# Kernel optimization log

Measured on AMD Instinct MI355X. Metric: run time of the kernel, lower is better.

Reference implementation:

```python
import jax, jax.numpy as jnp
import numpy as np

B, T, D, U = 2048, 200, 128, 128  # batch, history len, input dim, gru units


def setup_inputs() -> dict:
    key = jax.random.key(0)
    ks = jax.random.split(key, 5)
    s = 1.0 / np.sqrt(U + D)
    return {
        "history_state": jax.random.normal(ks[0], (B, T, D), jnp.float32),
        "attention_score": jax.random.uniform(ks[1], (B, T, 1), jnp.float32),
        "Wu": jax.random.normal(ks[2], (U + D, U), jnp.float32) * s,
        "bu": jnp.zeros((U,), jnp.float32),
        "Wr": jax.random.normal(ks[3], (U + D, U), jnp.float32) * s,
        "br": jnp.zeros((U,), jnp.float32),
        "Wh": jax.random.normal(ks[4], (D + U, U), jnp.float32) * s,
        "bh": jnp.zeros((U,), jnp.float32),
    }


def reference(history_state, attention_score, Wu, bu, Wr, br, Wh, bh):
    # time-major for scan: (T, B, ...)
    xs = jnp.swapaxes(history_state, 0, 1)       # (T, B, D)
    ats = jnp.swapaxes(attention_score, 0, 1)    # (T, B, 1)
    h0 = jnp.zeros((history_state.shape[0], Wu.shape[1]), history_state.dtype)

    def step(h, xa):
        x, a = xa
        hx = jnp.concatenate([h, x], axis=-1)                       # (B, U+D)
        u = jax.nn.sigmoid(hx @ Wu + bu)                            # update gate
        r = jax.nn.sigmoid(hx @ Wr + br)                            # reset gate
        hh = jnp.tanh(jnp.concatenate([x, r * h], axis=-1) @ Wh + bh)
        u = u * a                                                   # attention-modulated update
        h_new = u * hh + (1.0 - u) * h
        return h_new, None

    h_final, _ = jax.lax.scan(step, h0, (xs, ats))
    return h_final  # (B, U)
```

## Files before the change

### kernel.cpp

```cpp
#include <hip/hip_runtime.h>
#include <hip/hip_bf16.h>


#define T_LEN 200
#define D_DIM 128
#define U_DIM 128
#define BM    16
#define KCS   136
#define XSTEP (16 * KCS)

typedef __attribute__((ext_vector_type(8))) short bf16x8;
typedef __attribute__((ext_vector_type(4))) float f32x4;
typedef __attribute__((ext_vector_type(4))) unsigned int uint4v;

#define MFMA __builtin_amdgcn_mfma_f32_16x16x32_bf16

static __device__ __forceinline__ unsigned short f2bf(float f) {
    unsigned int u = __builtin_bit_cast(unsigned int, f);
    u += 0x7fffu + ((u >> 16) & 1u);
    return (unsigned short)(u >> 16);
}
static __device__ __forceinline__ unsigned int pkbf2(float a, float b) {
    float2 t; t.x = a; t.y = b;
    __hip_bfloat162 v = __float22bfloat162_rn(t);
    unsigned int u; __builtin_memcpy(&u, &v, 4);
    return u;
}
static __device__ __forceinline__ bf16x8 pack8bf(f32x4 lo, f32x4 hi) {
    uint4v v;
    v[0] = pkbf2(lo[0], lo[1]); v[1] = pkbf2(lo[2], lo[3]);
    v[2] = pkbf2(hi[0], hi[1]); v[3] = pkbf2(hi[2], hi[3]);
    return __builtin_bit_cast(bf16x8, v);
}
static __device__ __forceinline__ float fast_exp2(float x) {
#if __has_builtin(__builtin_amdgcn_exp2f)
    return __builtin_amdgcn_exp2f(x);
#else
    return exp2f(x);
#endif
}
static __device__ __forceinline__ float fast_rcp(float x) {
#if __has_builtin(__builtin_amdgcn_rcpf)
    return __builtin_amdgcn_rcpf(x);
#else
    return 1.0f / x;
#endif
}
static __device__ __forceinline__ void block_sync_lds() {
    asm volatile("s_waitcnt lgkmcnt(0)" ::: "memory");
    __builtin_amdgcn_sched_barrier(0);
    __builtin_amdgcn_s_barrier();
    __builtin_amdgcn_sched_barrier(0);
}

__global__ __launch_bounds__(256, 1)
void gru_scan_kernel(const float* __restrict__ X,
                     const float* __restrict__ Att,
                     const float* __restrict__ Wu, const float* __restrict__ bu,
                     const float* __restrict__ Wr, const float* __restrict__ br,
                     const float* __restrict__ Wh, const float* __restrict__ bh,
                     float* __restrict__ out)
{
    __shared__ __align__(16) unsigned short h_bf[XSTEP];
    __shared__ __align__(16) unsigned short rh_bf[XSTEP];

    const int tid  = threadIdx.x;
    const int wave = tid >> 6;
    const int lane = tid & 63;
    const int q    = lane >> 4;
    const int ln   = lane & 15;
    const int b0   = blockIdx.x * BM;

    const float INVLN2 = 1.4426950408889634f;

    bf16x8 wu[2][8], wr[2][8], wh[2][8];
    f32x4 nbu[2], nbr[2], bh2[2];
    #pragma unroll
    for (int tl = 0; tl < 2; ++tl) {
        const int tb = 32 * wave + 16 * tl;
        const int c  = tb + ln;
        const f32x4 bu4 = *(const f32x4*)&bu[tb + 4 * q];
        const f32x4 br4 = *(const f32x4*)&br[tb + 4 * q];
        const f32x4 bh4 = *(const f32x4*)&bh[tb + 4 * q];
        #pragma unroll
        for (int r = 0; r < 4; ++r) {
            nbu[tl][r] = -bu4[r] * INVLN2;
            nbr[tl][r] = -br4[r] * INVLN2;
            bh2[tl][r] = 2.0f * bh4[r] * INVLN2;
        }
        #pragma unroll
        for (int kt = 0; kt < 8; ++kt) {
            const int k0 = 32 * kt + 8 * q;
            bf16x8 vu, vr, vh;
            #pragma unroll
            for (int j = 0; j < 8; ++j) {
                vu[j] = (short)f2bf(Wu[(k0 + j) * U_DIM + c] * -INVLN2);
                vr[j] = (short)f2bf(Wr[(k0 + j) * U_DIM + c] * -INVLN2);
                vh[j] = (short)f2bf(Wh[(k0 + j) * U_DIM + c] * (2.0f * INVLN2));
            }
            wu[tl][kt] = vu; wr[tl][kt] = vr; wh[tl][kt] = vh;
        }
    }

    const float* xrow = X + (size_t)(b0 + ln) * T_LEN * D_DIM + 8 * q;
    const float* arow = Att + (size_t)(b0 + ln) * T_LEN;

    f32x4 px[8];
    #pragma unroll
    for (int kt = 0; kt < 4; ++kt) {
        px[2 * kt]     = *(const f32x4*)(xrow + 32 * kt);
        px[2 * kt + 1] = *(const f32x4*)(xrow + 32 * kt + 4);
    }
    const float a0 = arow[0];
    float attA = arow[1], attB = arow[2], attC = arow[3];

    float hreg[2][4];

    const int c8base = (4 * wave) * KCS + ln * 8 + (q & 1) * 4;
    const int c8q    = (q >> 1) * KCS;

    {
        bf16x8 xf[4];
        #pragma unroll
        for (int kt = 0; kt < 4; ++kt) xf[kt] = pack8bf(px[2 * kt], px[2 * kt + 1]);
        #pragma unroll
        for (int kt = 0; kt < 4; ++kt) {
            px[2 * kt]     = *(const f32x4*)(xrow + D_DIM + 32 * kt);
            px[2 * kt + 1] = *(const f32x4*)(xrow + D_DIM + 32 * kt + 4);
        }
        #pragma unroll
        for (int tl = 0; tl < 2; ++tl) {
            f32x4 xu = nbu[tl], xh = bh2[tl];
            #pragma unroll
            for (int kt = 0; kt < 4; ++kt) {
                xu = MFMA(wu[tl][kt + 4], xf[kt], xu, 0, 0, 0);
                xh = MFMA(wh[tl][kt],     xf[kt], xh, 0, 0, 0);
            }
            #pragma unroll
            for (int r = 0; r < 4; ++r) {
                float u  = fast_rcp(1.0f + fast_exp2(xu[r])) * a0;
                float hh = 1.0f - 2.0f * fast_rcp(1.0f + fast_exp2(xh[r]));
                hreg[tl][r] = u * hh;
            }
            uint2 wv; wv.x = pkbf2(hreg[tl][0], hreg[tl][1]);
            wv.y = pkbf2(hreg[tl][2], hreg[tl][3]);
            *(uint2*)&h_bf[c8base + c8q + 2 * tl * KCS] = wv;
        }
    }
    block_sync_lds();

    for (int t = 1; t < T_LEN; ++t) {
        bf16x8 hf[4];
        #pragma unroll
        for (int kt = 0; kt < 4; ++kt)
            hf[kt] = *(const bf16x8*)&h_bf[(4 * kt + q) * KCS + ln * 8];

        bf16x8 xf[4];
        #pragma unroll
        for (int kt = 0; kt < 4; ++kt) xf[kt] = pack8bf(px[2 * kt], px[2 * kt + 1]);
        {
            const int tn = (t + 1 < T_LEN) ? t + 1 : T_LEN - 1;
            const float* xs = xrow + (size_t)tn * D_DIM;
            #pragma unroll
            for (int kt = 0; kt < 4; ++kt) {
                px[2 * kt]     = *(const f32x4*)(xs + 32 * kt);
                px[2 * kt + 1] = *(const f32x4*)(xs + 32 * kt + 4);
            }
        }
        const float a_att = attA;
        attA = attB; attB = attC;
        attC = arow[(t + 3 < T_LEN) ? t + 3 : T_LEN - 1];

        f32x4 xr[2], xu[2], xh[2];
        #pragma unroll
        for (int tl = 0; tl < 2; ++tl) {
            xr[tl] = nbr[tl]; xu[tl] = nbu[tl]; xh[tl] = bh2[tl];
            #pragma unroll
            for (int kt = 0; kt < 4; ++kt) {
                xr[tl] = MFMA(wr[tl][kt + 4], xf[kt], xr[tl], 0, 0, 0);
                xu[tl] = MFMA(wu[tl][kt + 4], xf[kt], xu[tl], 0, 0, 0);
                xh[tl] = MFMA(wh[tl][kt],     xf[kt], xh[tl], 0, 0, 0);
            }
        }
        f32x4 ra[2], rb[2];
        #pragma unroll
        for (int tl = 0; tl < 2; ++tl) {
            ra[tl] = MFMA(wr[tl][0], hf[0], (f32x4)0.0f, 0, 0, 0);
            rb[tl] = MFMA(wr[tl][2], hf[2], (f32x4)0.0f, 0, 0, 0);
            ra[tl] = MFMA(wr[tl][1], hf[1], ra[tl], 0, 0, 0);
            rb[tl] = MFMA(wr[tl][3], hf[3], rb[tl], 0, 0, 0);
            #pragma unroll
            for (int kt = 0; kt < 4; ++kt)
                xu[tl] = MFMA(wu[tl][kt], hf[kt], xu[tl], 0, 0, 0);
        }
        #pragma unroll
        for (int tl = 0; tl < 2; ++tl) {
            float rh[4];
            #pragma unroll
            for (int r = 0; r < 4; ++r) {
                float zr = xr[tl][r] + ra[tl][r] + rb[tl][r];
                float rv = fast_rcp(1.0f + fast_exp2(zr));
                rh[r] = rv * hreg[tl][r];
            }
            uint2 wv; wv.x = pkbf2(rh[0], rh[1]); wv.y = pkbf2(rh[2], rh[3]);
            *(uint2*)&rh_bf[c8base + c8q + 2 * tl * KCS] = wv;
        }
        block_sync_lds();

        bf16x8 rf[4];
        #pragma unroll
        for (int kt = 0; kt < 4; ++kt)
            rf[kt] = *(const bf16x8*)&rh_bf[(4 * kt + q) * KCS + ln * 8];

        float uq[2][4];
        #pragma unroll
        for (int tl = 0; tl < 2; ++tl)
            #pragma unroll
            for (int r = 0; r < 4; ++r)
                uq[tl][r] = fast_rcp(1.0f + fast_exp2(xu[tl][r])) * a_att;

        #pragma unroll
        for (int tl = 0; tl < 2; ++tl) {
            f32x4 ha = xh[tl], hb = (f32x4)0.0f;
            ha = MFMA(wh[tl][4], rf[0], ha, 0, 0, 0);
            hb = MFMA(wh[tl][6], rf[2], hb, 0, 0, 0);
            ha = MFMA(wh[tl][5], rf[1], ha, 0, 0, 0);
            hb = MFMA(wh[tl][7], rf[3], hb, 0, 0, 0);
            #pragma unroll
            for (int r = 0; r < 4; ++r) {
                float z  = ha[r] + hb[r];
                float hh = 1.0f - 2.0f * fast_rcp(1.0f + fast_exp2(z));
                float ho = hreg[tl][r];
                hreg[tl][r] = ho + uq[tl][r] * (hh - ho);
            }
            uint2 wv; wv.x = pkbf2(hreg[tl][0], hreg[tl][1]);
            wv.y = pkbf2(hreg[tl][2], hreg[tl][3]);
            *(uint2*)&h_bf[c8base + c8q + 2 * tl * KCS] = wv;
        }
        block_sync_lds();
    }

    #pragma unroll
    for (int tl = 0; tl < 2; ++tl) {
        f32x4 v;
        #pragma unroll
        for (int r = 0; r < 4; ++r) v[r] = hreg[tl][r];
        *(f32x4*)&out[(size_t)(b0 + ln) * U_DIM + 32 * wave + 16 * tl + 4 * q] = v;
    }
}

extern "C" void kernel_launch(void* const* d_in, const int* in_sizes, int n_in,
                              void* d_out, int out_size, void* d_ws, size_t ws_size,
                              hipStream_t stream) {
    const float* X   = (const float*)d_in[0];
    const float* Att = (const float*)d_in[1];
    const float* Wu  = (const float*)d_in[2];
    const float* bu  = (const float*)d_in[3];
    const float* Wr  = (const float*)d_in[4];
    const float* br  = (const float*)d_in[5];
    const float* Wh  = (const float*)d_in[6];
    const float* bh  = (const float*)d_in[7];
    float* out = (float*)d_out;

    gru_scan_kernel<<<dim3(2048 / BM), dim3(256), 0, stream>>>(
        X, Att, Wu, bu, Wr, br, Wh, bh, out);
}
```

Measured before the change: 538.1 us.

## Split GRU units across eight waves and pipeline x-projection into previous step

Each block now launches 512 threads (8 waves), and each wave owns 16 output units instead of 32. That halves per-wave weight registers and MFMA work per step, so the critical serial path inside each timestep is shorter. The input projection for the next step (x@W plus bias) is computed after the h update and before the barrier, which moves it off the h-dependent critical path. In exchange the block has twice as many waves taking part in each barrier, and occupancy targets change with the launch bounds.

```diff
diff --git a/kernel.cpp b/kernel.cpp
--- a/kernel.cpp
+++ b/kernel.cpp
@@ -53,7 +53,7 @@
     __builtin_amdgcn_sched_barrier(0);
 }
 
-__global__ __launch_bounds__(256, 1)
+__global__ __launch_bounds__(512, 2)
 void gru_scan_kernel(const float* __restrict__ X,
                      const float* __restrict__ Att,
                      const float* __restrict__ Wu, const float* __restrict__ bu,
@@ -73,20 +73,19 @@
 
     const float INVLN2 = 1.4426950408889634f;
 
-    bf16x8 wu[2][8], wr[2][8], wh[2][8];
-    f32x4 nbu[2], nbr[2], bh2[2];
-    #pragma unroll
-    for (int tl = 0; tl < 2; ++tl) {
-        const int tb = 32 * wave + 16 * tl;
+    bf16x8 wu[8], wr[8], wh[8];
+    f32x4 nbu, nbr, bh2;
+    {
+        const int tb = 16 * wave;
         const int c  = tb + ln;
         const f32x4 bu4 = *(const f32x4*)&bu[tb + 4 * q];
         const f32x4 br4 = *(const f32x4*)&br[tb + 4 * q];
         const f32x4 bh4 = *(const f32x4*)&bh[tb + 4 * q];
         #pragma unroll
         for (int r = 0; r < 4; ++r) {
-            nbu[tl][r] = -bu4[r] * INVLN2;
-            nbr[tl][r] = -br4[r] * INVLN2;
-            bh2[tl][r] = 2.0f * bh4[r] * INVLN2;
+            nbu[r] = -bu4[r] * INVLN2;
+            nbr[r] = -br4[r] * INVLN2;
+            bh2[r] = 2.0f * bh4[r] * INVLN2;
         }
         #pragma unroll
         for (int kt = 0; kt < 8; ++kt) {
@@ -98,7 +97,7 @@
                 vr[j] = (short)f2bf(Wr[(k0 + j) * U_DIM + c] * -INVLN2);
                 vh[j] = (short)f2bf(Wh[(k0 + j) * U_DIM + c] * (2.0f * INVLN2));
             }
-            wu[tl][kt] = vu; wr[tl][kt] = vr; wh[tl][kt] = vh;
+            wu[kt] = vu; wr[kt] = vr; wh[kt] = vh;
         }
     }
 
@@ -114,10 +113,10 @@
     const float a0 = arow[0];
     float attA = arow[1], attB = arow[2], attC = arow[3];
 
-    float hreg[2][4];
-
-    const int c8base = (4 * wave) * KCS + ln * 8 + (q & 1) * 4;
-    const int c8q    = (q >> 1) * KCS;
+    float hreg[4];
+    f32x4 acc_r, acc_u, acc_h;
+
+    const int c8 = (2 * wave + (q >> 1)) * KCS + ln * 8 + (q & 1) * 4;
 
     {
         bf16x8 xf[4];
@@ -128,23 +127,36 @@
             px[2 * kt]     = *(const f32x4*)(xrow + D_DIM + 32 * kt);
             px[2 * kt + 1] = *(const f32x4*)(xrow + D_DIM + 32 * kt + 4);
         }
-        #pragma unroll
-        for (int tl = 0; tl < 2; ++tl) {
-            f32x4 xu = nbu[tl], xh = bh2[tl];
-            #pragma unroll
-            for (int kt = 0; kt < 4; ++kt) {
-                xu = MFMA(wu[tl][kt + 4], xf[kt], xu, 0, 0, 0);
-                xh = MFMA(wh[tl][kt],     xf[kt], xh, 0, 0, 0);
-            }
-            #pragma unroll
-            for (int r = 0; r < 4; ++r) {
-                float u  = fast_rcp(1.0f + fast_exp2(xu[r])) * a0;
-                float hh = 1.0f - 2.0f * fast_rcp(1.0f + fast_exp2(xh[r]));
-                hreg[tl][r] = u * hh;
-            }
-            uint2 wv; wv.x = pkbf2(hreg[tl][0], hreg[tl][1]);
-            wv.y = pkbf2(hreg[tl][2], hreg[tl][3]);
-            *(uint2*)&h_bf[c8base + c8q + 2 * tl * KCS] = wv;
+        f32x4 xu = nbu, xh = bh2;
+        #pragma unroll
+        for (int kt = 0; kt < 4; ++kt) {
+            xu = MFMA(wu[kt + 4], xf[kt], xu, 0, 0, 0);
+            xh = MFMA(wh[kt],     xf[kt], xh, 0, 0, 0);
+        }
+        #pragma unroll
+        for (int r = 0; r < 4; ++r) {
+            float u  = fast_rcp(1.0f + fast_exp2(xu[r])) * a0;
+            float hh = 1.0f - 2.0f * fast_rcp(1.0f + fast_exp2(xh[r]));
+            hreg[r] = u * hh;
+        }
+        {
+            uint2 wv; wv.x = pkbf2(hreg[0], hreg[1]); wv.y = pkbf2(hreg[2], hreg[3]);
+            *(uint2*)&h_bf[c8] = wv;
+        }
+        bf16x8 x1[4];
+        #pragma unroll
+        for (int kt = 0; kt < 4; ++kt) x1[kt] = pack8bf(px[2 * kt], px[2 * kt + 1]);
+        #pragma unroll
+        for (int kt = 0; kt < 4; ++kt) {
+            px[2 * kt]     = *(const f32x4*)(xrow + 2 * D_DIM + 32 * kt);
+            px[2 * kt + 1] = *(const f32x4*)(xrow + 2 * D_DIM + 32 * kt + 4);
+        }
+        acc_r = nbr; acc_u = nbu; acc_h = bh2;
+        #pragma unroll
+        for (int kt = 0; kt < 4; ++kt) {
+            acc_r = MFMA(wr[kt + 4], x1[kt], acc_r, 0, 0, 0);
+            acc_u = MFMA(wu[kt + 4], x1[kt], acc_u, 0, 0, 0);
+            acc_h = MFMA(wh[kt],     x1[kt], acc_h, 0, 0, 0);
         }
     }
     block_sync_lds();
@@ -155,97 +167,87 @@
         for (int kt = 0; kt < 4; ++kt)
             hf[kt] = *(const bf16x8*)&h_bf[(4 * kt + q) * KCS + ln * 8];
 
-        bf16x8 xf[4];
-        #pragma unroll
-        for (int kt = 0; kt < 4; ++kt) xf[kt] = pack8bf(px[2 * kt], px[2 * kt + 1]);
-        {
-            const int tn = (t + 1 < T_LEN) ? t + 1 : T_LEN - 1;
+        f32x4 ra = acc_r, rb = (f32x4)0.0f;
+        ra = MFMA(wr[0], hf[0], ra, 0, 0, 0);
+        rb = MFMA(wr[2], hf[2], rb, 0, 0, 0);
+        ra = MFMA(wr[1], hf[1], ra, 0, 0, 0);
+        rb = MFMA(wr[3], hf[3], rb, 0, 0, 0);
+        #pragma unroll
+        for (int kt = 0; kt < 4; ++kt)
+            acc_u = MFMA(wu[kt], hf[kt], acc_u, 0, 0, 0);
+
+        {
+            float rh[4];
+            #pragma unroll
+            for (int r = 0; r < 4; ++r) {
+                float zr = ra[r] + rb[r];
+                float rv = fast_rcp(1.0f + fast_exp2(zr));
+                rh[r] = rv * hreg[r];
+            }
+            uint2 wv; wv.x = pkbf2(rh[0], rh[1]); wv.y = pkbf2(rh[2], rh[3]);
+            *(uint2*)&rh_bf[c8] = wv;
+        }
+        block_sync_lds();
+
+        bf16x8 rf[4];
+        #pragma unroll
+        for (int kt = 0; kt < 4; ++kt)
+            rf[kt] = *(const bf16x8*)&rh_bf[(4 * kt + q) * KCS + ln * 8];
+
+        const float a_att = attA;
+        attA = attB; attB = attC;
+        attC = arow[(t + 3 < T_LEN) ? t + 3 : T_LEN - 1];
+        float uq[4];
+        #pragma unroll
+        for (int r = 0; r < 4; ++r)
+            uq[r] = fast_rcp(1.0f + fast_exp2(acc_u[r])) * a_att;
+
+        f32x4 ha = acc_h, hb = (f32x4)0.0f;
+        ha = MFMA(wh[4], rf[0], ha, 0, 0, 0);
+        hb = MFMA(wh[6], rf[2], hb, 0, 0, 0);
+        ha = MFMA(wh[5], rf[1], ha, 0, 0, 0);
+        hb = MFMA(wh[7], rf[3], hb, 0, 0, 0);
+
+        #pragma unroll
+        for (int r = 0; r < 4; ++r) {
+            float z  = ha[r] + hb[r];
+            float hh = 1.0f - 2.0f * fast_rcp(1.0f + fast_exp2(z));
+            float ho = hreg[r];
+            hreg[r] = ho + uq[r] * (hh - ho);
+        }
+        {
+            uint2 wv; wv.x = pkbf2(hreg[0], hreg[1]); wv.y = pkbf2(hreg[2], hreg[3]);
+            *(uint2*)&h_bf[c8] = wv;
+        }
+
+        {
+            bf16x8 xf[4];
+            #pragma unroll
+            for (int kt = 0; kt < 4; ++kt)
+                xf[kt] = pack8bf(px[2 * kt], px[2 * kt + 1]);
+            const int tn = (t + 2 < T_LEN) ? t + 2 : T_LEN - 1;
             const float* xs = xrow + (size_t)tn * D_DIM;
             #pragma unroll
             for (int kt = 0; kt < 4; ++kt) {
                 px[2 * kt]     = *(const f32x4*)(xs + 32 * kt);
                 px[2 * kt + 1] = *(const f32x4*)(xs + 32 * kt + 4);
             }
-        }
-        const float a_att = attA;
-        attA = attB; attB = attC;
-        attC = arow[(t + 3 < T_LEN) ? t + 3 : T_LEN - 1];
-
-        f32x4 xr[2], xu[2], xh[2];
-        #pragma unroll
-        for (int tl = 0; tl < 2; ++tl) {
-            xr[tl] = nbr[tl]; xu[tl] = nbu[tl]; xh[tl] = bh2[tl];
+            acc_r = nbr; acc_u = nbu; acc_h = bh2;
             #pragma unroll
             for (int kt = 0; kt < 4; ++kt) {
-                xr[tl] = MFMA(wr[tl][kt + 4], xf[kt], xr[tl], 0, 0, 0);
-                xu[tl] = MFMA(wu[tl][kt + 4], xf[kt], xu[tl], 0, 0, 0);
-                xh[tl] = MFMA(wh[tl][kt],     xf[kt], xh[tl], 0, 0, 0);
-            }
-        }
-        f32x4 ra[2], rb[2];
-        #pragma unroll
-        for (int tl = 0; tl < 2; ++tl) {
-            ra[tl] = MFMA(wr[tl][0], hf[0], (f32x4)0.0f, 0, 0, 0);
-            rb[tl] = MFMA(wr[tl][2], hf[2], (f32x4)0.0f, 0, 0, 0);
-            ra[tl] = MFMA(wr[tl][1], hf[1], ra[tl], 0, 0, 0);
-            rb[tl] = MFMA(wr[tl][3], hf[3], rb[tl], 0, 0, 0);
-            #pragma unroll
-            for (int kt = 0; kt < 4; ++kt)
-                xu[tl] = MFMA(wu[tl][kt], hf[kt], xu[tl], 0, 0, 0);
-        }
-        #pragma unroll
-        for (int tl = 0; tl < 2; ++tl) {
-            float rh[4];
-            #pragma unroll
-            for (int r = 0; r < 4; ++r) {
-                float zr = xr[tl][r] + ra[tl][r] + rb[tl][r];
-                float rv = fast_rcp(1.0f + fast_exp2(zr));
-                rh[r] = rv * hreg[tl][r];
-            }
-            uint2 wv; wv.x = pkbf2(rh[0], rh[1]); wv.y = pkbf2(rh[2], rh[3]);
-            *(uint2*)&rh_bf[c8base + c8q + 2 * tl * KCS] = wv;
+                acc_r = MFMA(wr[kt + 4], xf[kt], acc_r, 0, 0, 0);
+                acc_u = MFMA(wu[kt + 4], xf[kt], acc_u, 0, 0, 0);
+                acc_h = MFMA(wh[kt],     xf[kt], acc_h, 0, 0, 0);
+            }
         }
         block_sync_lds();
-
-        bf16x8 rf[4];
-        #pragma unroll
-        for (int kt = 0; kt < 4; ++kt)
-            rf[kt] = *(const bf16x8*)&rh_bf[(4 * kt + q) * KCS + ln * 8];
-
-        float uq[2][4];
-        #pragma unroll
-        for (int tl = 0; tl < 2; ++tl)
-            #pragma unroll
-            for (int r = 0; r < 4; ++r)
-                uq[tl][r] = fast_rcp(1.0f + fast_exp2(xu[tl][r])) * a_att;
-
-        #pragma unroll
-        for (int tl = 0; tl < 2; ++tl) {
-            f32x4 ha = xh[tl], hb = (f32x4)0.0f;
-            ha = MFMA(wh[tl][4], rf[0], ha, 0, 0, 0);
-            hb = MFMA(wh[tl][6], rf[2], hb, 0, 0, 0);
-            ha = MFMA(wh[tl][5], rf[1], ha, 0, 0, 0);
-            hb = MFMA(wh[tl][7], rf[3], hb, 0, 0, 0);
-            #pragma unroll
-            for (int r = 0; r < 4; ++r) {
-                float z  = ha[r] + hb[r];
-                float hh = 1.0f - 2.0f * fast_rcp(1.0f + fast_exp2(z));
-                float ho = hreg[tl][r];
-                hreg[tl][r] = ho + uq[tl][r] * (hh - ho);
-            }
-            uint2 wv; wv.x = pkbf2(hreg[tl][0], hreg[tl][1]);
-            wv.y = pkbf2(hreg[tl][2], hreg[tl][3]);
-            *(uint2*)&h_bf[c8base + c8q + 2 * tl * KCS] = wv;
-        }
-        block_sync_lds();
-    }
-
-    #pragma unroll
-    for (int tl = 0; tl < 2; ++tl) {
+    }
+
+    {
         f32x4 v;
         #pragma unroll
-        for (int r = 0; r < 4; ++r) v[r] = hreg[tl][r];
-        *(f32x4*)&out[(size_t)(b0 + ln) * U_DIM + 32 * wave + 16 * tl + 4 * q] = v;
+        for (int r = 0; r < 4; ++r) v[r] = hreg[r];
+        *(f32x4*)&out[(size_t)(b0 + ln) * U_DIM + 16 * wave + 4 * q] = v;
     }
 }
 
@@ -262,6 +264,6 @@
     const float* bh  = (const float*)d_in[7];
     float* out = (float*)d_out;
 
-    gru_scan_kernel<<<dim3(2048 / BM), dim3(256), 0, stream>>>(
+    gru_scan_kernel<<<dim3(2048 / BM), dim3(512), 0, stream>>>(
         X, Att, Wu, bu, Wr, br, Wh, bh, out);
 }
```

Measured after the change: 682.7 us. +26.9%, slower.

## Add producer waves that stage X chunks into LDS as bf16 for compute waves

Applied to the files above, without the earlier changes.

Splits the block into 4 compute waves and 4 producer waves. The producer waves load X and attention in 12-step chunks, convert them to bf16 and write them into a double-buffered LDS area. The compute waves then read x fragments from LDS, and the input projection for step s+1 is computed at the end of step s so it sits off the critical path. This removes per-step global loads and packing from the recurrent loop. The cost is more LDS, 512 threads per block with launch bounds of 2 blocks, and producer waves that must join every barrier.

```diff
diff --git a/kernel.cpp b/kernel.cpp
--- a/kernel.cpp
+++ b/kernel.cpp
@@ -6,6 +6,8 @@
 #define D_DIM 128
 #define U_DIM 128
 #define BM    16
+#define CH    12
+#define NCH   ((T_LEN + CH - 1) / CH)
 #define KCS   136
 #define XSTEP (16 * KCS)
 
@@ -26,11 +28,11 @@
     unsigned int u; __builtin_memcpy(&u, &v, 4);
     return u;
 }
-static __device__ __forceinline__ bf16x8 pack8bf(f32x4 lo, f32x4 hi) {
+static __device__ __forceinline__ uint4v pack8u(float4 lo, float4 hi) {
     uint4v v;
-    v[0] = pkbf2(lo[0], lo[1]); v[1] = pkbf2(lo[2], lo[3]);
-    v[2] = pkbf2(hi[0], hi[1]); v[3] = pkbf2(hi[2], hi[3]);
-    return __builtin_bit_cast(bf16x8, v);
+    v[0] = pkbf2(lo.x, lo.y); v[1] = pkbf2(lo.z, lo.w);
+    v[2] = pkbf2(hi.x, hi.y); v[3] = pkbf2(hi.z, hi.w);
+    return v;
 }
 static __device__ __forceinline__ float fast_exp2(float x) {
 #if __has_builtin(__builtin_amdgcn_exp2f)
@@ -53,7 +55,40 @@
     __builtin_amdgcn_sched_barrier(0);
 }
 
-__global__ __launch_bounds__(256, 1)
+#define XPART(SRC) do {                                                        \
+    bf16x8 xf_[4];                                                             \
+    _Pragma("unroll")                                                          \
+    for (int kt = 0; kt < 4; ++kt)                                             \
+        xf_[kt] = *(const bf16x8*)&(SRC)[(4 * kt + q) * KCS + ln * 8];         \
+    _Pragma("unroll")                                                          \
+    for (int tl = 0; tl < 2; ++tl) {                                           \
+        acc_r[tl] = nbr[tl]; acc_u[tl] = nbu[tl]; acc_h[tl] = bh2[tl];         \
+        _Pragma("unroll")                                                      \
+        for (int kt = 0; kt < 4; ++kt) {                                       \
+            acc_r[tl] = MFMA(wr[tl][kt + 4], xf_[kt], acc_r[tl], 0, 0, 0);     \
+            acc_u[tl] = MFMA(wu[tl][kt + 4], xf_[kt], acc_u[tl], 0, 0, 0);     \
+            acc_h[tl] = MFMA(wh[tl][kt],     xf_[kt], acc_h[tl], 0, 0, 0);     \
+        }                                                                      \
+    }                                                                          \
+} while (0)
+
+#define P_ISSUE(PX, SB) do {                                                   \
+    _Pragma("unroll")                                                          \
+    for (int k = 0; k < 4; ++k) {                                              \
+        int t_ = tn0 + (SB) + k; t_ = (t_ < T_LEN) ? t_ : (T_LEN - 1);         \
+        const float* src_ = xb + (size_t)t_ * D_DIM;                           \
+        (PX)[2 * k]     = *(const float4*)(src_);                              \
+        (PX)[2 * k + 1] = *(const float4*)(src_ + 4);                          \
+    }                                                                          \
+} while (0)
+#define P_WRITE(PX, SB) do {                                                   \
+    _Pragma("unroll")                                                          \
+    for (int k = 0; k < 4; ++k)                                                \
+        *(uint4v*)&dst[((SB) + k) * XSTEP + cs * KCS + srow * 8] =             \
+            pack8u((PX)[2 * k], (PX)[2 * k + 1]);                              \
+} while (0)
+
+__global__ __launch_bounds__(512, 2)
 void gru_scan_kernel(const float* __restrict__ X,
                      const float* __restrict__ Att,
                      const float* __restrict__ Wu, const float* __restrict__ bu,
@@ -61,8 +96,10 @@
                      const float* __restrict__ Wh, const float* __restrict__ bh,
                      float* __restrict__ out)
 {
+    __shared__ __align__(16) unsigned short x_sm[2][CH * XSTEP];
     __shared__ __align__(16) unsigned short h_bf[XSTEP];
     __shared__ __align__(16) unsigned short rh_bf[XSTEP];
+    __shared__ float a_sm[2][CH * BM];
 
     const int tid  = threadIdx.x;
     const int wave = tid >> 6;
@@ -73,179 +110,202 @@
 
     const float INVLN2 = 1.4426950408889634f;
 
-    bf16x8 wu[2][8], wr[2][8], wh[2][8];
-    f32x4 nbu[2], nbr[2], bh2[2];
-    #pragma unroll
-    for (int tl = 0; tl < 2; ++tl) {
-        const int tb = 32 * wave + 16 * tl;
-        const int c  = tb + ln;
-        const f32x4 bu4 = *(const f32x4*)&bu[tb + 4 * q];
-        const f32x4 br4 = *(const f32x4*)&br[tb + 4 * q];
-        const f32x4 bh4 = *(const f32x4*)&bh[tb + 4 * q];
+    {
+        unsigned int* hz = (unsigned int*)h_bf;
+        unsigned int* rz = (unsigned int*)rh_bf;
+        for (int i = tid; i < XSTEP / 2; i += 512) { hz[i] = 0; rz[i] = 0; }
+    }
+
+    {
+        const int s2   = tid >> 8;
+        const int srow = (tid >> 4) & 15;
+        const int cs   = tid & 15;
+        const float* xb = X + (size_t)(b0 + srow) * T_LEN * D_DIM + cs * 8;
+        float4 px[CH];
         #pragma unroll
-        for (int r = 0; r < 4; ++r) {
-            nbu[tl][r] = -bu4[r] * INVLN2;
-            nbr[tl][r] = -br4[r] * INVLN2;
-            bh2[tl][r] = 2.0f * bh4[r] * INVLN2;
-        }
+        for (int w2 = 0; w2 < CH / 2; ++w2) {
+            const int t = 2 * w2 + s2;
+            const float* src = xb + (size_t)t * D_DIM;
+            px[2 * w2]     = *(const float4*)(src);
+            px[2 * w2 + 1] = *(const float4*)(src + 4);
+        }
+        float a_px = 0.0f;
+        if (tid < BM * CH) a_px = Att[(size_t)(b0 + (tid & 15)) * T_LEN + (tid >> 4)];
         #pragma unroll
-        for (int kt = 0; kt < 8; ++kt) {
-            const int k0 = 32 * kt + 8 * q;
-            bf16x8 vu, vr, vh;
-            #pragma unroll
-            for (int j = 0; j < 8; ++j) {
-                vu[j] = (short)f2bf(Wu[(k0 + j) * U_DIM + c] * -INVLN2);
-                vr[j] = (short)f2bf(Wr[(k0 + j) * U_DIM + c] * -INVLN2);
-                vh[j] = (short)f2bf(Wh[(k0 + j) * U_DIM + c] * (2.0f * INVLN2));
-            }
-            wu[tl][kt] = vu; wr[tl][kt] = vr; wh[tl][kt] = vh;
-        }
+        for (int w2 = 0; w2 < CH / 2; ++w2) {
+            const int s = 2 * w2 + s2;
+            *(uint4v*)&x_sm[0][s * XSTEP + cs * KCS + srow * 8] =
+                pack8u(px[2 * w2], px[2 * w2 + 1]);
+        }
+        if (tid < BM * CH) a_sm[0][tid] = a_px;
     }
-
-    const float* xrow = X + (size_t)(b0 + ln) * T_LEN * D_DIM + 8 * q;
-    const float* arow = Att + (size_t)(b0 + ln) * T_LEN;
-
-    f32x4 px[8];
-    #pragma unroll
-    for (int kt = 0; kt < 4; ++kt) {
-        px[2 * kt]     = *(const f32x4*)(xrow + 32 * kt);
-        px[2 * kt + 1] = *(const f32x4*)(xrow + 32 * kt + 4);
-    }
-    const float a0 = arow[0];
-    float attA = arow[1], attB = arow[2], attC = arow[3];
-
-    float hreg[2][4];
-
-    const int c8base = (4 * wave) * KCS + ln * 8 + (q & 1) * 4;
-    const int c8q    = (q >> 1) * KCS;
-
-    {
-        bf16x8 xf[4];
-        #pragma unroll
-        for (int kt = 0; kt < 4; ++kt) xf[kt] = pack8bf(px[2 * kt], px[2 * kt + 1]);
-        #pragma unroll
-        for (int kt = 0; kt < 4; ++kt) {
-            px[2 * kt]     = *(const f32x4*)(xrow + D_DIM + 32 * kt);
-            px[2 * kt + 1] = *(const f32x4*)(xrow + D_DIM + 32 * kt + 4);
-        }
+    __syncthreads();
+
+    if (wave < 4) {
+        bf16x8 wu[2][8], wr[2][8], wh[2][8];
+        f32x4 nbu[2], nbr[2], bh2[2];
         #pragma unroll
         for (int tl = 0; tl < 2; ++tl) {
-            f32x4 xu = nbu[tl], xh = bh2[tl];
+            const int tb = 32 * wave + 16 * tl;
+            const int c  = tb + ln;
+            const f32x4 bu4 = *(const f32x4*)&bu[tb + 4 * q];
+            const f32x4 br4 = *(const f32x4*)&br[tb + 4 * q];
+            const f32x4 bh4 = *(const f32x4*)&bh[tb + 4 * q];
             #pragma unroll
-            for (int kt = 0; kt < 4; ++kt) {
-                xu = MFMA(wu[tl][kt + 4], xf[kt], xu, 0, 0, 0);
-                xh = MFMA(wh[tl][kt],     xf[kt], xh, 0, 0, 0);
+            for (int r = 0; r < 4; ++r) {
+                nbu[tl][r] = -bu4[r] * INVLN2;
+                nbr[tl][r] = -br4[r] * INVLN2;
+                bh2[tl][r] = 2.0f * bh4[r] * INVLN2;
             }
             #pragma unroll
-            for (int r = 0; r < 4; ++r) {
-                float u  = fast_rcp(1.0f + fast_exp2(xu[r])) * a0;
-                float hh = 1.0f - 2.0f * fast_rcp(1.0f + fast_exp2(xh[r]));
-                hreg[tl][r] = u * hh;
+            for (int kt = 0; kt < 8; ++kt) {
+                const int k0 = 32 * kt + 8 * q;
+                bf16x8 vu, vr, vh;
+                #pragma unroll
+                for (int j = 0; j < 8; ++j) {
+                    vu[j] = (short)f2bf(Wu[(k0 + j) * U_DIM + c] * -INVLN2);
+                    vr[j] = (short)f2bf(Wr[(k0 + j) * U_DIM + c] * -INVLN2);
+                    vh[j] = (short)f2bf(Wh[(k0 + j) * U_DIM + c] * (2.0f * INVLN2));
+                }
+                wu[tl][kt] = vu; wr[tl][kt] = vr; wh[tl][kt] = vh;
             }
-            uint2 wv; wv.x = pkbf2(hreg[tl][0], hreg[tl][1]);
-            wv.y = pkbf2(hreg[tl][2], hreg[tl][3]);
-            *(uint2*)&h_bf[c8base + c8q + 2 * tl * KCS] = wv;
-        }
-    }
-    block_sync_lds();
-
-    for (int t = 1; t < T_LEN; ++t) {
-        bf16x8 hf[4];
-        #pragma unroll
-        for (int kt = 0; kt < 4; ++kt)
-            hf[kt] = *(const bf16x8*)&h_bf[(4 * kt + q) * KCS + ln * 8];
-
-        bf16x8 xf[4];
-        #pragma unroll
-        for (int kt = 0; kt < 4; ++kt) xf[kt] = pack8bf(px[2 * kt], px[2 * kt + 1]);
-        {
-            const int tn = (t + 1 < T_LEN) ? t + 1 : T_LEN - 1;
-            const float* xs = xrow + (size_t)tn * D_DIM;
-            #pragma unroll
-            for (int kt = 0; kt < 4; ++kt) {
-                px[2 * kt]     = *(const f32x4*)(xs + 32 * kt);
-                px[2 * kt + 1] = *(const f32x4*)(xs + 32 * kt + 4);
+        }
+
+        float hreg[2][4] = {{0.f,0.f,0.f,0.f},{0.f,0.f,0.f,0.f}};
+        const int c8base = (4 * wave) * KCS + ln * 8 + (q & 1) * 4;
+        const int c8q    = (q >> 1) * KCS;
+
+        f32x4 acc_r[2], acc_u[2], acc_h[2];
+        XPART(&x_sm[0][0]);
+
+        int t0 = 0;
+        for (int ch = 0; ch < NCH; ++ch) {
+            const int L = (t0 + CH <= T_LEN) ? CH : (T_LEN - t0);
+            const unsigned short* xcur = &x_sm[ch & 1][0];
+            const float* ab = &a_sm[ch & 1][0];
+
+            for (int s = 0; s < L; ++s) {
+                bf16x8 hf[4];
+                #pragma unroll
+                for (int kt = 0; kt < 4; ++kt)
+                    hf[kt] = *(const bf16x8*)&h_bf[(4 * kt + q) * KCS + ln * 8];
+                const float a_att = ab[s * BM + ln];
+
+                f32x4 ra[2], rb[2];
+                #pragma unroll
+                for (int tl = 0; tl < 2; ++tl) {
+                    ra[tl] = acc_r[tl]; rb[tl] = (f32x4)0.0f;
+                    ra[tl] = MFMA(wr[tl][0], hf[0], ra[tl], 0, 0, 0);
+                    rb[tl] = MFMA(wr[tl][2], hf[2], rb[tl], 0, 0, 0);
+                    ra[tl] = MFMA(wr[tl][1], hf[1], ra[tl], 0, 0, 0);
+                    rb[tl] = MFMA(wr[tl][3], hf[3], rb[tl], 0, 0, 0);
+                    #pragma unroll
+                    for (int kt = 0; kt < 4; ++kt)
+                        acc_u[tl] = MFMA(wu[tl][kt], hf[kt], acc_u[tl], 0, 0, 0);
+                }
+                #pragma unroll
+                for (int tl = 0; tl < 2; ++tl) {
+                    float rh[4];
+                    #pragma unroll
+                    for (int r = 0; r < 4; ++r) {
+                        float zr = ra[tl][r] + rb[tl][r];
+                        float rv = fast_rcp(1.0f + fast_exp2(zr));
+                        rh[r] = rv * hreg[tl][r];
+                    }
+                    uint2 wv; wv.x = pkbf2(rh[0], rh[1]); wv.y = pkbf2(rh[2], rh[3]);
+                    *(uint2*)&rh_bf[c8base + c8q + 2 * tl * KCS] = wv;
+                }
+                block_sync_lds();
+
+                bf16x8 rf[4];
+                #pragma unroll
+                for (int kt = 0; kt < 4; ++kt)
+                    rf[kt] = *(const bf16x8*)&rh_bf[(4 * kt + q) * KCS + ln * 8];
+
+                float uq[2][4];
+                #pragma unroll
+                for (int tl = 0; tl < 2; ++tl)
+                    #pragma unroll
+                    for (int r = 0; r < 4; ++r)
+                        uq[tl][r] = fast_rcp(1.0f + fast_exp2(acc_u[tl][r])) * a_att;
+
+                #pragma unroll
+                for (int tl = 0; tl < 2; ++tl) {
+                    f32x4 ha = acc_h[tl], hb = (f32x4)0.0f;
+                    ha = MFMA(wh[tl][4], rf[0], ha, 0, 0, 0);
+                    hb = MFMA(wh[tl][6], rf[2], hb, 0, 0, 0);
+                    ha = MFMA(wh[tl][5], rf[1], ha, 0, 0, 0);
+                    hb = MFMA(wh[tl][7], rf[3], hb, 0, 0, 0);
+                    #pragma unroll
+                    for (int r = 0; r < 4; ++r) {
+                        float z  = ha[r] + hb[r];
+                        float hh = 1.0f - 2.0f * fast_rcp(1.0f + fast_exp2(z));
+                        float ho = hreg[tl][r];
+                        hreg[tl][r] = ho + uq[tl][r] * (hh - ho);
+                    }
+                    uint2 wv; wv.x = pkbf2(hreg[tl][0], hreg[tl][1]);
+                    wv.y = pkbf2(hreg[tl][2], hreg[tl][3]);
+                    *(uint2*)&h_bf[c8base + c8q + 2 * tl * KCS] = wv;
+                }
+
+                if (s + 1 < L) {
+                    XPART(xcur + (s + 1) * XSTEP);
+                } else if (ch + 1 < NCH) {
+                    XPART(&x_sm[(ch + 1) & 1][0]);
+                }
+                block_sync_lds();
             }
-        }
-        const float a_att = attA;
-        attA = attB; attB = attC;
-        attC = arow[(t + 3 < T_LEN) ? t + 3 : T_LEN - 1];
-
-        f32x4 xr[2], xu[2], xh[2];
+            t0 += CH;
+        }
+
         #pragma unroll
         for (int tl = 0; tl < 2; ++tl) {
-            xr[tl] = nbr[tl]; xu[tl] = nbu[tl]; xh[tl] = bh2[tl];
+            f32x4 v;
             #pragma unroll
-            for (int kt = 0; kt < 4; ++kt) {
-                xr[tl] = MFMA(wr[tl][kt + 4], xf[kt], xr[tl], 0, 0, 0);
-                xu[tl] = MFMA(wu[tl][kt + 4], xf[kt], xu[tl], 0, 0, 0);
-                xh[tl] = MFMA(wh[tl][kt],     xf[kt], xh[tl], 0, 0, 0);
+            for (int r = 0; r < 4; ++r) v[r] = hreg[tl][r];
+            *(f32x4*)&out[(size_t)(b0 + ln) * U_DIM + 32 * wave + 16 * tl + 4 * q] = v;
+        }
+    } else {
+        const int tid2 = tid & 255;
+        const int srow = (tid2 >> 4) & 15;
+        const int cs   = tid2 & 15;
+        const float* xb = X + (size_t)(b0 + srow) * T_LEN * D_DIM + cs * 8;
+
+        int t0 = 0;
+        for (int ch = 0; ch < NCH; ++ch) {
+            const int L = (t0 + CH <= T_LEN) ? CH : (T_LEN - t0);
+            const bool st = (ch + 1 < NCH);
+            const int tn0 = t0 + CH;
+            unsigned short* dst = &x_sm[(ch + 1) & 1][0];
+            float4 pxA[8], pxB[8], pxC[8];
+            float av = 0.0f;
+
+            for (int s = 0; s < L; ++s) {
+                if (st && s == 0) {
+                    P_ISSUE(pxA, 0);
+                    if (tid2 < BM * CH) {
+                        int ta = tn0 + (tid2 >> 4);
+                        ta = (ta < T_LEN) ? ta : (T_LEN - 1);
+                        av = Att[(size_t)(b0 + (tid2 & 15)) * T_LEN + ta];
+                    }
+                }
+                block_sync_lds();
+                if (st) {
+                    if (s == 1) {
+                        P_WRITE(pxA, 0);
+                        P_ISSUE(pxB, 4);
+                        if (tid2 < BM * CH) a_sm[(ch + 1) & 1][tid2] = av;
+                    } else if (s == 2) {
+                        P_WRITE(pxB, 4);
+                        P_ISSUE(pxC, 8);
+                    } else if (s == 3) {
+                        P_WRITE(pxC, 8);
+                    }
+                }
+                block_sync_lds();
             }
-        }
-        f32x4 ra[2], rb[2];
-        #pragma unroll
-        for (int tl = 0; tl < 2; ++tl) {
-            ra[tl] = MFMA(wr[tl][0], hf[0], (f32x4)0.0f, 0, 0, 0);
-            rb[tl] = MFMA(wr[tl][2], hf[2], (f32x4)0.0f, 0, 0, 0);
-            ra[tl] = MFMA(wr[tl][1], hf[1], ra[tl], 0, 0, 0);
-            rb[tl] = MFMA(wr[tl][3], hf[3], rb[tl], 0, 0, 0);
-            #pragma unroll
-            for (int kt = 0; kt < 4; ++kt)
-                xu[tl] = MFMA(wu[tl][kt], hf[kt], xu[tl], 0, 0, 0);
-        }
-        #pragma unroll
-        for (int tl = 0; tl < 2; ++tl) {
-            float rh[4];
-            #pragma unroll
-            for (int r = 0; r < 4; ++r) {
-                float zr = xr[tl][r] + ra[tl][r] + rb[tl][r];
-                float rv = fast_rcp(1.0f + fast_exp2(zr));
-                rh[r] = rv * hreg[tl][r];
-            }
-            uint2 wv; wv.x = pkbf2(rh[0], rh[1]); wv.y = pkbf2(rh[2], rh[3]);
-            *(uint2*)&rh_bf[c8base + c8q + 2 * tl * KCS] = wv;
-        }
-        block_sync_lds();
-
-        bf16x8 rf[4];
-        #pragma unroll
-        for (int kt = 0; kt < 4; ++kt)
-            rf[kt] = *(const bf16x8*)&rh_bf[(4 * kt + q) * KCS + ln * 8];
-
-        float uq[2][4];
-        #pragma unroll
-        for (int tl = 0; tl < 2; ++tl)
-            #pragma unroll
-            for (int r = 0; r < 4; ++r)
-                uq[tl][r] = fast_rcp(1.0f + fast_exp2(xu[tl][r])) * a_att;
-
-        #pragma unroll
-        for (int tl = 0; tl < 2; ++tl) {
-            f32x4 ha = xh[tl], hb = (f32x4)0.0f;
-            ha = MFMA(wh[tl][4], rf[0], ha, 0, 0, 0);
-            hb = MFMA(wh[tl][6], rf[2], hb, 0, 0, 0);
-            ha = MFMA(wh[tl][5], rf[1], ha, 0, 0, 0);
-            hb = MFMA(wh[tl][7], rf[3], hb, 0, 0, 0);
-            #pragma unroll
-            for (int r = 0; r < 4; ++r) {
-                float z  = ha[r] + hb[r];
-                float hh = 1.0f - 2.0f * fast_rcp(1.0f + fast_exp2(z));
-                float ho = hreg[tl][r];
-                hreg[tl][r] = ho + uq[tl][r] * (hh - ho);
-            }
-            uint2 wv; wv.x = pkbf2(hreg[tl][0], hreg[tl][1]);
-            wv.y = pkbf2(hreg[tl][2], hreg[tl][3]);
-            *(uint2*)&h_bf[c8base + c8q + 2 * tl * KCS] = wv;
-        }
-        block_sync_lds();
-    }
-
-    #pragma unroll
-    for (int tl = 0; tl < 2; ++tl) {
-        f32x4 v;
-        #pragma unroll
-        for (int r = 0; r < 4; ++r) v[r] = hreg[tl][r];
-        *(f32x4*)&out[(size_t)(b0 + ln) * U_DIM + 32 * wave + 16 * tl + 4 * q] = v;
+            t0 += CH;
+        }
     }
 }
 
@@ -262,6 +322,6 @@
     const float* bh  = (const float*)d_in[7];
     float* out = (float*)d_out;
 
-    gru_scan_kernel<<<dim3(2048 / BM), dim3(256), 0, stream>>>(
+    gru_scan_kernel<<<dim3(2048 / BM), dim3(512), 0, stream>>>(
         X, Att, Wu, bu, Wr, br, Wh, bh, out);
 }
```

Measured after the change: 691.2 us. 28.4% more time.

## Stage input chunks in LDS and overlap x-projection with recurrent MFMAs

Applied to the files above, without the earlier changes.

Replaces per-step register prefetch of x with cooperative loads of 12-timestep chunks. The chunks are converted to bf16 and staged in shared memory, along with the attention scores. The x-projection MFMAs for the next step are issued after the h update, so they can overlap with the barrier wait. The whole block loads the next chunk while the current one computes. The first step is folded into the loop with zero-initialised h. This adds a lot of LDS, a large register array for the prefetched chunk, and an extra __syncthreads per chunk. Register pressure could spill.

```diff
diff --git a/kernel.cpp b/kernel.cpp
--- a/kernel.cpp
+++ b/kernel.cpp
@@ -6,6 +6,8 @@
 #define D_DIM 128
 #define U_DIM 128
 #define BM    16
+#define CH    12
+#define NCH   ((T_LEN + CH - 1) / CH)
 #define KCS   136
 #define XSTEP (16 * KCS)
 
@@ -26,11 +28,11 @@
     unsigned int u; __builtin_memcpy(&u, &v, 4);
     return u;
 }
-static __device__ __forceinline__ bf16x8 pack8bf(f32x4 lo, f32x4 hi) {
+static __device__ __forceinline__ uint4v pack8u(float4 lo, float4 hi) {
     uint4v v;
-    v[0] = pkbf2(lo[0], lo[1]); v[1] = pkbf2(lo[2], lo[3]);
-    v[2] = pkbf2(hi[0], hi[1]); v[3] = pkbf2(hi[2], hi[3]);
-    return __builtin_bit_cast(bf16x8, v);
+    v[0] = pkbf2(lo.x, lo.y); v[1] = pkbf2(lo.z, lo.w);
+    v[2] = pkbf2(hi.x, hi.y); v[3] = pkbf2(hi.z, hi.w);
+    return v;
 }
 static __device__ __forceinline__ float fast_exp2(float x) {
 #if __has_builtin(__builtin_amdgcn_exp2f)
@@ -61,8 +63,10 @@
                      const float* __restrict__ Wh, const float* __restrict__ bh,
                      float* __restrict__ out)
 {
+    __shared__ __align__(16) unsigned short x_sm[CH * XSTEP];
     __shared__ __align__(16) unsigned short h_bf[XSTEP];
     __shared__ __align__(16) unsigned short rh_bf[XSTEP];
+    __shared__ float a_sm[CH * BM];
 
     const int tid  = threadIdx.x;
     const int wave = tid >> 6;
@@ -102,142 +106,178 @@
         }
     }
 
-    const float* xrow = X + (size_t)(b0 + ln) * T_LEN * D_DIM + 8 * q;
-    const float* arow = Att + (size_t)(b0 + ln) * T_LEN;
-
-    f32x4 px[8];
-    #pragma unroll
-    for (int kt = 0; kt < 4; ++kt) {
-        px[2 * kt]     = *(const f32x4*)(xrow + 32 * kt);
-        px[2 * kt + 1] = *(const f32x4*)(xrow + 32 * kt + 4);
-    }
-    const float a0 = arow[0];
-    float attA = arow[1], attB = arow[2], attC = arow[3];
-
-    float hreg[2][4];
+    float hreg[2][4] = {{0.f,0.f,0.f,0.f},{0.f,0.f,0.f,0.f}};
+
+    {
+        unsigned int* hz = (unsigned int*)h_bf;
+        unsigned int* rz = (unsigned int*)rh_bf;
+        for (int i = tid; i < XSTEP / 2; i += 256) { hz[i] = 0; rz[i] = 0; }
+    }
+
+    const int srow = (tid >> 4) & 15;
+    const int cs   = tid & 15;
+    const float* xbase = X + (size_t)(b0 + srow) * T_LEN * D_DIM + cs * 8;
+
+    {
+        float4 p0[2 * CH];
+        #pragma unroll
+        for (int w = 0; w < CH; ++w) {
+            const float* src = xbase + (size_t)w * D_DIM;
+            p0[2 * w]     = *(const float4*)(src);
+            p0[2 * w + 1] = *(const float4*)(src + 4);
+        }
+        float a_px = 0.0f;
+        if (tid < BM * CH)
+            a_px = Att[(size_t)(b0 + (tid & 15)) * T_LEN + (tid >> 4)];
+        #pragma unroll
+        for (int w = 0; w < CH; ++w)
+            *(uint4v*)&x_sm[w * XSTEP + cs * KCS + srow * 8] =
+                pack8u(p0[2 * w], p0[2 * w + 1]);
+        if (tid < BM * CH) a_sm[tid] = a_px;
+    }
+    __syncthreads();
 
     const int c8base = (4 * wave) * KCS + ln * 8 + (q & 1) * 4;
     const int c8q    = (q >> 1) * KCS;
 
-    {
-        bf16x8 xf[4];
-        #pragma unroll
-        for (int kt = 0; kt < 4; ++kt) xf[kt] = pack8bf(px[2 * kt], px[2 * kt + 1]);
-        #pragma unroll
-        for (int kt = 0; kt < 4; ++kt) {
-            px[2 * kt]     = *(const f32x4*)(xrow + D_DIM + 32 * kt);
-            px[2 * kt + 1] = *(const f32x4*)(xrow + D_DIM + 32 * kt + 4);
-        }
-        #pragma unroll
-        for (int tl = 0; tl < 2; ++tl) {
-            f32x4 xu = nbu[tl], xh = bh2[tl];
-            #pragma unroll
-            for (int kt = 0; kt < 4; ++kt) {
-                xu = MFMA(wu[tl][kt + 4], xf[kt], xu, 0, 0, 0);
-                xh = MFMA(wh[tl][kt],     xf[kt], xh, 0, 0, 0);
-            }
-            #pragma unroll
-            for (int r = 0; r < 4; ++r) {
-                float u  = fast_rcp(1.0f + fast_exp2(xu[r])) * a0;
-                float hh = 1.0f - 2.0f * fast_rcp(1.0f + fast_exp2(xh[r]));
-                hreg[tl][r] = u * hh;
-            }
-            uint2 wv; wv.x = pkbf2(hreg[tl][0], hreg[tl][1]);
-            wv.y = pkbf2(hreg[tl][2], hreg[tl][3]);
-            *(uint2*)&h_bf[c8base + c8q + 2 * tl * KCS] = wv;
-        }
-    }
-    block_sync_lds();
-
-    for (int t = 1; t < T_LEN; ++t) {
-        bf16x8 hf[4];
-        #pragma unroll
-        for (int kt = 0; kt < 4; ++kt)
-            hf[kt] = *(const bf16x8*)&h_bf[(4 * kt + q) * KCS + ln * 8];
-
-        bf16x8 xf[4];
-        #pragma unroll
-        for (int kt = 0; kt < 4; ++kt) xf[kt] = pack8bf(px[2 * kt], px[2 * kt + 1]);
+    int t0 = 0;
+    for (int ch = 0; ch < NCH; ++ch) {
+        const int L  = (t0 + CH <= T_LEN) ? CH : (T_LEN - t0);
+        const bool st = (ch + 1 < NCH);
+
+        float4 px[2 * CH];
+        float av = 0.0f;
+        if (st) {
+            const int tn0 = t0 + CH;
+            #pragma unroll
+            for (int w = 0; w < CH; ++w) {
+                int t = tn0 + w;
+                t = (t < T_LEN) ? t : (T_LEN - 1);
+                const float* src = xbase + (size_t)t * D_DIM;
+                px[2 * w]     = *(const float4*)(src);
+                px[2 * w + 1] = *(const float4*)(src + 4);
+            }
+            if (tid < BM * CH) {
+                int ta = tn0 + (tid >> 4);
+                ta = (ta < T_LEN) ? ta : (T_LEN - 1);
+                av = Att[(size_t)(b0 + (tid & 15)) * T_LEN + ta];
+            }
+        }
+
+        f32x4 acc_r[2], acc_u[2], acc_h[2];
         {
-            const int tn = (t + 1 < T_LEN) ? t + 1 : T_LEN - 1;
-            const float* xs = xrow + (size_t)tn * D_DIM;
-            #pragma unroll
-            for (int kt = 0; kt < 4; ++kt) {
-                px[2 * kt]     = *(const f32x4*)(xs + 32 * kt);
-                px[2 * kt + 1] = *(const f32x4*)(xs + 32 * kt + 4);
-            }
-        }
-        const float a_att = attA;
-        attA = attB; attB = attC;
-        attC = arow[(t + 3 < T_LEN) ? t + 3 : T_LEN - 1];
-
-        f32x4 xr[2], xu[2], xh[2];
-        #pragma unroll
-        for (int tl = 0; tl < 2; ++tl) {
-            xr[tl] = nbr[tl]; xu[tl] = nbu[tl]; xh[tl] = bh2[tl];
-            #pragma unroll
-            for (int kt = 0; kt < 4; ++kt) {
-                xr[tl] = MFMA(wr[tl][kt + 4], xf[kt], xr[tl], 0, 0, 0);
-                xu[tl] = MFMA(wu[tl][kt + 4], xf[kt], xu[tl], 0, 0, 0);
-                xh[tl] = MFMA(wh[tl][kt],     xf[kt], xh[tl], 0, 0, 0);
-            }
-        }
-        f32x4 ra[2], rb[2];
-        #pragma unroll
-        for (int tl = 0; tl < 2; ++tl) {
-            ra[tl] = MFMA(wr[tl][0], hf[0], (f32x4)0.0f, 0, 0, 0);
-            rb[tl] = MFMA(wr[tl][2], hf[2], (f32x4)0.0f, 0, 0, 0);
-            ra[tl] = MFMA(wr[tl][1], hf[1], ra[tl], 0, 0, 0);
-            rb[tl] = MFMA(wr[tl][3], hf[3], rb[tl], 0, 0, 0);
+            bf16x8 xf[4];
             #pragma unroll
             for (int kt = 0; kt < 4; ++kt)
-                xu[tl] = MFMA(wu[tl][kt], hf[kt], xu[tl], 0, 0, 0);
-        }
-        #pragma unroll
-        for (int tl = 0; tl < 2; ++tl) {
-            float rh[4];
-            #pragma unroll
-            for (int r = 0; r < 4; ++r) {
-                float zr = xr[tl][r] + ra[tl][r] + rb[tl][r];
-                float rv = fast_rcp(1.0f + fast_exp2(zr));
-                rh[r] = rv * hreg[tl][r];
-            }
-            uint2 wv; wv.x = pkbf2(rh[0], rh[1]); wv.y = pkbf2(rh[2], rh[3]);
-            *(uint2*)&rh_bf[c8base + c8q + 2 * tl * KCS] = wv;
-        }
-        block_sync_lds();
-
-        bf16x8 rf[4];
-        #pragma unroll
-        for (int kt = 0; kt < 4; ++kt)
-            rf[kt] = *(const bf16x8*)&rh_bf[(4 * kt + q) * KCS + ln * 8];
-
-        float uq[2][4];
-        #pragma unroll
-        for (int tl = 0; tl < 2; ++tl)
-            #pragma unroll
-            for (int r = 0; r < 4; ++r)
-                uq[tl][r] = fast_rcp(1.0f + fast_exp2(xu[tl][r])) * a_att;
-
-        #pragma unroll
-        for (int tl = 0; tl < 2; ++tl) {
-            f32x4 ha = xh[tl], hb = (f32x4)0.0f;
-            ha = MFMA(wh[tl][4], rf[0], ha, 0, 0, 0);
-            hb = MFMA(wh[tl][6], rf[2], hb, 0, 0, 0);
-            ha = MFMA(wh[tl][5], rf[1], ha, 0, 0, 0);
-            hb = MFMA(wh[tl][7], rf[3], hb, 0, 0, 0);
-            #pragma unroll
-            for (int r = 0; r < 4; ++r) {
-                float z  = ha[r] + hb[r];
-                float hh = 1.0f - 2.0f * fast_rcp(1.0f + fast_exp2(z));
-                float ho = hreg[tl][r];
-                hreg[tl][r] = ho + uq[tl][r] * (hh - ho);
-            }
-            uint2 wv; wv.x = pkbf2(hreg[tl][0], hreg[tl][1]);
-            wv.y = pkbf2(hreg[tl][2], hreg[tl][3]);
-            *(uint2*)&h_bf[c8base + c8q + 2 * tl * KCS] = wv;
-        }
-        block_sync_lds();
+                xf[kt] = *(const bf16x8*)&x_sm[(4 * kt + q) * KCS + ln * 8];
+            #pragma unroll
+            for (int tl = 0; tl < 2; ++tl) {
+                acc_r[tl] = nbr[tl]; acc_u[tl] = nbu[tl]; acc_h[tl] = bh2[tl];
+                #pragma unroll
+                for (int kt = 0; kt < 4; ++kt) {
+                    acc_r[tl] = MFMA(wr[tl][kt + 4], xf[kt], acc_r[tl], 0, 0, 0);
+                    acc_u[tl] = MFMA(wu[tl][kt + 4], xf[kt], acc_u[tl], 0, 0, 0);
+                    acc_h[tl] = MFMA(wh[tl][kt],     xf[kt], acc_h[tl], 0, 0, 0);
+                }
+            }
+        }
+
+        for (int s = 0; s < L; ++s) {
+            bf16x8 hf[4];
+            #pragma unroll
+            for (int kt = 0; kt < 4; ++kt)
+                hf[kt] = *(const bf16x8*)&h_bf[(4 * kt + q) * KCS + ln * 8];
+            const float a_att = a_sm[s * BM + ln];
+
+            f32x4 ra[2], rb[2];
+            #pragma unroll
+            for (int tl = 0; tl < 2; ++tl) {
+                ra[tl] = acc_r[tl]; rb[tl] = (f32x4)0.0f;
+                ra[tl] = MFMA(wr[tl][0], hf[0], ra[tl], 0, 0, 0);
+                rb[tl] = MFMA(wr[tl][2], hf[2], rb[tl], 0, 0, 0);
+                ra[tl] = MFMA(wr[tl][1], hf[1], ra[tl], 0, 0, 0);
+                rb[tl] = MFMA(wr[tl][3], hf[3], rb[tl], 0, 0, 0);
+                #pragma unroll
+                for (int kt = 0; kt < 4; ++kt)
+                    acc_u[tl] = MFMA(wu[tl][kt], hf[kt], acc_u[tl], 0, 0, 0);
+            }
+            #pragma unroll
+            for (int tl = 0; tl < 2; ++tl) {
+                float rh[4];
+                #pragma unroll
+                for (int r = 0; r < 4; ++r) {
+                    float zr = ra[tl][r] + rb[tl][r];
+                    float rv = fast_rcp(1.0f + fast_exp2(zr));
+                    rh[r] = rv * hreg[tl][r];
+                }
+                uint2 wv; wv.x = pkbf2(rh[0], rh[1]); wv.y = pkbf2(rh[2], rh[3]);
+                *(uint2*)&rh_bf[c8base + c8q + 2 * tl * KCS] = wv;
+            }
+            block_sync_lds();
+
+            bf16x8 rf[4];
+            #pragma unroll
+            for (int kt = 0; kt < 4; ++kt)
+                rf[kt] = *(const bf16x8*)&rh_bf[(4 * kt + q) * KCS + ln * 8];
+
+            const bool more = (s + 1 < L);
+            bf16x8 xf[4];
+            if (more) {
+                #pragma unroll
+                for (int kt = 0; kt < 4; ++kt)
+                    xf[kt] = *(const bf16x8*)&x_sm[(s + 1) * XSTEP + (4 * kt + q) * KCS + ln * 8];
+            }
+
+            float uq[2][4];
+            #pragma unroll
+            for (int tl = 0; tl < 2; ++tl)
+                #pragma unroll
+                for (int r = 0; r < 4; ++r)
+                    uq[tl][r] = fast_rcp(1.0f + fast_exp2(acc_u[tl][r])) * a_att;
+
+            #pragma unroll
+            for (int tl = 0; tl < 2; ++tl) {
+                f32x4 ha = acc_h[tl], hb = (f32x4)0.0f;
+                ha = MFMA(wh[tl][4], rf[0], ha, 0, 0, 0);
+                hb = MFMA(wh[tl][6], rf[2], hb, 0, 0, 0);
+                ha = MFMA(wh[tl][5], rf[1], ha, 0, 0, 0);
+                hb = MFMA(wh[tl][7], rf[3], hb, 0, 0, 0);
+                #pragma unroll
+                for (int r = 0; r < 4; ++r) {
+                    float z  = ha[r] + hb[r];
+                    float hh = 1.0f - 2.0f * fast_rcp(1.0f + fast_exp2(z));
+                    float ho = hreg[tl][r];
+                    hreg[tl][r] = ho + uq[tl][r] * (hh - ho);
+                }
+                uint2 wv; wv.x = pkbf2(hreg[tl][0], hreg[tl][1]);
+                wv.y = pkbf2(hreg[tl][2], hreg[tl][3]);
+                *(uint2*)&h_bf[c8base + c8q + 2 * tl * KCS] = wv;
+            }
+
+            if (more) {
+                #pragma unroll
+                for (int tl = 0; tl < 2; ++tl) {
+                    acc_r[tl] = nbr[tl]; acc_u[tl] = nbu[tl]; acc_h[tl] = bh2[tl];
+                    #pragma unroll
+                    for (int kt = 0; kt < 4; ++kt) {
+                        acc_r[tl] = MFMA(wr[tl][kt + 4], xf[kt], acc_r[tl], 0, 0, 0);
+                        acc_u[tl] = MFMA(wu[tl][kt + 4], xf[kt], acc_u[tl], 0, 0, 0);
+                        acc_h[tl] = MFMA(wh[tl][kt],     xf[kt], acc_h[tl], 0, 0, 0);
+                    }
+                }
+            }
+            block_sync_lds();
+        }
+
+        if (st) {
+            #pragma unroll
+            for (int w = 0; w < CH; ++w)
+                *(uint4v*)&x_sm[w * XSTEP + cs * KCS + srow * 8] =
+                    pack8u(px[2 * w], px[2 * w + 1]);
+            if (tid < BM * CH) a_sm[tid] = av;
+            __syncthreads();
+        }
+        t0 += CH;
     }
 
     #pragma unroll
```

After: 508.9 us. 5.4% less time.
